# Kernel optimization log

Hardware: AMD Instinct MI355X
Metric: run time of the kernel (lower is better)

Reference implementation:

```python
import jax, jax.numpy as jnp
import numpy as np

N_HEAD = 8
N_HB_TERM = 3


def setup_inputs() -> dict:
    key = jax.random.key(0)
    ks = jax.random.split(key, 6)
    B, N, C, T = 8, 4096, 512, 4096
    s = 0.02  # weight init scale
    return {
        "x": jax.random.normal(ks[0], (B, N, C), jnp.float32),
        "y": jax.random.normal(ks[1], (N_HB_TERM, B, T, C), jnp.float32),
        "Wq": jax.random.normal(ks[2], (C, C), jnp.float32) * s,
        "bq": jnp.zeros((C,), jnp.float32),
        "Wk": jax.random.normal(ks[3], (N_HB_TERM, C, C), jnp.float32) * s,
        "bk": jnp.zeros((N_HB_TERM, C), jnp.float32),
        "Wv": jax.random.normal(ks[4], (N_HB_TERM, C, C), jnp.float32) * s,
        "bv": jnp.zeros((N_HB_TERM, C), jnp.float32),
        "Wp": jax.random.normal(ks[5], (C, C), jnp.float32) * s,
        "bp": jnp.zeros((C,), jnp.float32),
    }


def _heads(t, B, T, H, d):
    # (B, T, C) -> (B, H, T, d)
    return t.reshape(B, T, H, d).transpose(0, 2, 1, 3)


def reference(x, y, Wq, bq, Wk, bk, Wv, bv, Wp, bp):
    B, N, C = x.shape
    H = N_HEAD
    d = C // H
    # query projection + softmax feature map over head dim
    q = _heads(x @ Wq.T + bq, B, N, H, d)          # (B,H,N,d)
    q = jax.nn.softmax(q, axis=-1)
    out = q  # faithful to original: out initialized to q
    for i in range(N_HB_TERM):
        yi = y[i]                                   # (B,T,C)
        T = yi.shape[1]
        k = _heads(yi @ Wk[i].T + bk[i], B, T, H, d)
        v = _heads(yi @ Wv[i].T + bv[i], B, T, H, d)
        k = jax.nn.softmax(k, axis=-1)
        k_cumsum = k.sum(axis=-2, keepdims=True)    # (B,H,1,d)
        D_inv = 1.0 / (q * k_cumsum).sum(axis=-1, keepdims=True)  # (B,H,N,1)
        ctx = jnp.einsum('bhtd,bhte->bhde', k, v)   # (B,H,d,d) small context
        out = out + jnp.einsum('bhnd,bhde->bhne', q, ctx) * D_inv
    out = out.transpose(0, 2, 1, 3).reshape(B, N, C)  # b h n d -> b n (h d)
    return out @ Wp.T + bp
```

## Files before the change

### kernel.cpp

```cpp
#include <hip/hip_runtime.h>


#define B_  8
#define N_  4096
#define C_  512
#define T_  4096
#define H_  8
#define M_  (B_*N_)

typedef __bf16 bf16_8 __attribute__((ext_vector_type(8)));
typedef __bf16 bf16_4 __attribute__((ext_vector_type(4)));
typedef float  f32_4  __attribute__((ext_vector_type(4)));

__device__ __forceinline__ unsigned short f2bf(float f) {
  unsigned u = __float_as_uint(f);
  unsigned r = 0x7FFFu + ((u >> 16) & 1u);
  return (unsigned short)((u + r) >> 16);
}

__device__ __forceinline__ void gload16(const void* g, void* l) {
  __builtin_amdgcn_global_load_lds(
      (const __attribute__((address_space(1))) unsigned int*)g,
      (__attribute__((address_space(3))) unsigned int*)l, 16, 0, 0);
}

__device__ __forceinline__ bf16_8 cvt8(float4 a, float4 b) {
  bf16_8 v;
  v[0]=(__bf16)a.x; v[1]=(__bf16)a.y; v[2]=(__bf16)a.z; v[3]=(__bf16)a.w;
  v[4]=(__bf16)b.x; v[5]=(__bf16)b.y; v[6]=(__bf16)b.z; v[7]=(__bf16)b.w;
  return v;
}

__global__ __launch_bounds__(256) void cvt_f32_bf16(
    const float* __restrict__ in, unsigned short* __restrict__ out, long n4)
{
  long i = (long)blockIdx.x * blockDim.x + threadIdx.x;
  long stride = (long)gridDim.x * blockDim.x;
  for (; i < n4; i += stride) {
    float4 v = ((const float4*)in)[i];
    ushort4 o;
    o.x = f2bf(v.x); o.y = f2bf(v.y); o.z = f2bf(v.z); o.w = f2bf(v.w);
    ((ushort4*)out)[i] = o;
  }
}

__global__ __launch_bounds__(256) void cvt_weights(
    const float* __restrict__ Wq, const float* __restrict__ Wk,
    const float* __restrict__ Wv, const float* __restrict__ Wp,
    unsigned short* __restrict__ wb)
{
  const size_t WCC = (size_t)C_*C_;
  const float* src; unsigned short* dst; long n4;
  switch (blockIdx.y) {
    case 0: src = Wq; dst = wb;         n4 = WCC/4;   break;
    case 1: src = Wk; dst = wb + WCC;   n4 = 3*WCC/4; break;
    case 2: src = Wv; dst = wb + 4*WCC; n4 = 3*WCC/4; break;
    default:src = Wp; dst = wb + 7*WCC; n4 = WCC/4;   break;
  }
  long i = (long)blockIdx.x * blockDim.x + threadIdx.x;
  long stride = (long)gridDim.x * blockDim.x;
  for (; i < n4; i += stride) {
    float4 v = ((const float4*)src)[i];
    ushort4 o;
    o.x = f2bf(v.x); o.y = f2bf(v.y); o.z = f2bf(v.z); o.w = f2bf(v.w);
    ((ushort4*)dst)[i] = o;
  }
}

template<int EPI, int ADT>
__global__ __launch_bounds__(256, 2) void gemm_all(
    const void* __restrict__ Av,
    const unsigned short* __restrict__ Bw,
    const float* __restrict__ bias,
    void* __restrict__ outp)
{
  __shared__ char smem[65536];

  const int tid = threadIdx.x, lane = tid & 63, wid = tid >> 6;
  const int wr = wid >> 1, wc = wid & 1;
  const int l15 = lane & 15, l16 = lane >> 4;
  const size_t row0 = (size_t)blockIdx.x * 128;
  const int col0 = blockIdx.y * 128;

  f32_4 acc[4][4] = {};
  float4 ra[4][2];

  auto load_a = [&](int k0) {
#pragma unroll
    for (int j = 0; j < 4; ++j) {
      int cc = j*256 + tid, row = cc >> 3, s = cc & 7;
      const float* src = (const float*)Av + (row0 + row)*512 + k0 + s*8;
      ra[j][0] = *(const float4*)src;
      ra[j][1] = *(const float4*)(src + 4);
    }
  };
  auto write_a = [&](int bsel) {
    unsigned short* dst = (unsigned short*)smem;
#pragma unroll
    for (int j = 0; j < 4; ++j) {
      int cc = j*256 + tid, row = cc >> 3, s = cc & 7;
      *(bf16_8*)&dst[bsel*8192 + row*64 + ((s ^ (row & 7)) << 3)] = cvt8(ra[j][0], ra[j][1]);
    }
  };
  auto stage_a16 = [&](int k0, int bsel) {
#pragma unroll
    for (int j = 0; j < 4; ++j) {
      int cc = j*256 + tid, row = cc >> 3, s = cc & 7;
      gload16((const unsigned short*)Av + (row0 + row)*512 + k0 + ((s ^ (row & 7)) << 3),
              smem + bsel*16384 + (size_t)(j*256 + wid*64)*16);
    }
  };
  auto stage_b = [&](int k0, int bsel) {
#pragma unroll
    for (int j = 0; j < 4; ++j) {
      int cc = j*256 + tid, row = cc >> 3, s = cc & 7;
      gload16(Bw + (size_t)(col0 + row)*512 + k0 + ((s ^ (row & 7)) << 3),
              smem + 32768 + bsel*16384 + (size_t)(j*256 + wid*64)*16);
    }
  };

  if constexpr (ADT == 0) { load_a(0); stage_b(0, 0); write_a(0); }
  else                    { stage_a16(0, 0); stage_b(0, 0); }
  __syncthreads();
  for (int t = 0; t < 8; ++t) {
    int cur = t & 1;
    if (t < 7) {
      if constexpr (ADT == 0) load_a((t+1)*64);
      else                    stage_a16((t+1)*64, cur ^ 1);
      stage_b((t+1)*64, cur ^ 1);
    }
    const unsigned short* sA = (const unsigned short*)(smem + cur*16384);
    const unsigned short* sB = (const unsigned short*)(smem + 32768 + cur*16384);
#pragma unroll
    for (int kk = 0; kk < 64; kk += 32) {
      bf16_8 af[4], bfr[4];
#pragma unroll
      for (int mi = 0; mi < 4; ++mi) {
        int r = wr*64 + mi*16 + l15;
        int ch = (kk >> 3) + l16;
        af[mi] = *(const bf16_8*)&sA[r*64 + ((ch ^ (r & 7)) << 3)];
      }
#pragma unroll
      for (int ni = 0; ni < 4; ++ni) {
        int r = wc*64 + ni*16 + l15;
        int ch = (kk >> 3) + l16;
        bfr[ni] = *(const bf16_8*)&sB[r*64 + ((ch ^ (r & 7)) << 3)];
      }
#pragma unroll
      for (int mi = 0; mi < 4; ++mi)
#pragma unroll
        for (int ni = 0; ni < 4; ++ni)
          acc[mi][ni] = __builtin_amdgcn_mfma_f32_16x16x32_bf16(af[mi], bfr[ni], acc[mi][ni], 0, 0, 0);
    }
    if (t < 7) { if constexpr (ADT == 0) write_a(cur ^ 1); }
    __syncthreads();
  }

  if constexpr (EPI == 0) {
    float* Cf = (float*)outp;
#pragma unroll
    for (int mi = 0; mi < 4; ++mi) {
      int rb = wr*64 + mi*16 + l16*4;
#pragma unroll
      for (int ni = 0; ni < 4; ++ni) {
        int col = col0 + wc*64 + ni*16 + l15;
        float bv = bias[col];
#pragma unroll
        for (int jj = 0; jj < 4; ++jj)
          Cf[(row0 + rb + jj)*512 + col] = acc[mi][ni][jj] + bv;
      }
    }
  } else {
    unsigned short* ob = (unsigned short*)outp;
    float bvv[4];
#pragma unroll
    for (int ni = 0; ni < 4; ++ni) bvv[ni] = bias[col0 + wc*64 + ni*16 + l15];
    unsigned short* sE = (unsigned short*)smem;
#pragma unroll
    for (int mi = 0; mi < 4; ++mi) {
#pragma unroll
      for (int jj = 0; jj < 4; ++jj) {
        float x[4];
        float s = 0.f;
#pragma unroll
        for (int ni = 0; ni < 4; ++ni) {
          x[ni] = __expf(acc[mi][ni][jj] + bvv[ni]);
          s += x[ni];
        }
#pragma unroll
        for (int o = 8; o; o >>= 1) s += __shfl_xor(s, o);
        float inv = 1.0f / s;
        int r = wr*64 + mi*16 + l16*4 + jj;
#pragma unroll
        for (int ni = 0; ni < 4; ++ni) {
          __bf16 h = (__bf16)(x[ni] * inv);
          sE[r*136 + wc*64 + ni*16 + l15] = *(unsigned short*)&h;
        }
      }
    }
    __syncthreads();
    int r = tid >> 1, seg = tid & 1;
    unsigned short* orow = ob + (row0 + r)*512 + col0 + seg*64;
#pragma unroll
    for (int u = 0; u < 8; ++u)
      *(uint4*)(orow + u*8) = *(const uint4*)&sE[r*136 + seg*64 + u*8];
  }
}

__global__ __launch_bounds__(256, 2) void kvctx_kernel(
    const unsigned short* __restrict__ yb_all,
    const unsigned short* __restrict__ wk_all,
    const unsigned short* __restrict__ wv_all,
    const float* __restrict__ bk_all,
    const float* __restrict__ bv_all,
    float* __restrict__ part,
    float* __restrict__ kcp)
{
  __shared__ char smem[65536];
  unsigned short* sKT = (unsigned short*)smem;
  unsigned short* sVT = (unsigned short*)(smem + 17408);

  const int tid = threadIdx.x, lane = tid & 63, wid = tid >> 6;
  const int wr = wid >> 1, wc = wid & 1;
  const int l15 = lane & 15, l16 = lane >> 4;
  const int gx = blockIdx.x, i = blockIdx.z;
  const int h = gx >> 6, bx = gx & 63;
  const int b = bx >> 3, sub = bx & 7;
  const int bh = b*8 + h;

  const unsigned short* yb = yb_all + (size_t)i*M_*512;
  const unsigned short* Wk_b = wk_all + (size_t)i*512*512 + (size_t)h*64*512;
  const unsigned short* Wv_b = wv_all + (size_t)i*512*512 + (size_t)h*64*512;
  const float* bk = bk_all + i*512 + h*64;
  const float* bv = bv_all + i*512 + h*64;

  f32_4 cacc[2][2] = {};
  float kcp_r[4] = {0.f, 0.f, 0.f, 0.f};

  for (int chunk = 0; chunk < 4; ++chunk) {
    const size_t row0 = (size_t)bx*512 + chunk*128;
    f32_4 acc[4][4] = {};

    auto stage = [&](int k0, int bsel) {
#pragma unroll
      for (int j = 0; j < 4; ++j) {
        int cc = j*256 + tid, row = cc >> 3, s = cc & 7;
        gload16(yb + (row0 + row)*512 + k0 + ((s ^ (row & 7)) << 3),
                smem + bsel*16384 + (size_t)(j*256 + wid*64)*16);
        const unsigned short* wsrc = (j < 2)
            ? Wk_b + (size_t)row*512
            : Wv_b + (size_t)(row - 64)*512;
        gload16(wsrc + k0 + ((s ^ (row & 7)) << 3),
                smem + 32768 + bsel*16384 + (size_t)(j*256 + wid*64)*16);
      }
    };

    stage(0, 0);
    __syncthreads();
    for (int t = 0; t < 8; ++t) {
      int cur = t & 1;
      if (t < 7) stage((t+1)*64, cur ^ 1);
      const unsigned short* sA = (const unsigned short*)(smem + cur*16384);
      const unsigned short* sB = (const unsigned short*)(smem + 32768 + cur*16384);
#pragma unroll
      for (int kk = 0; kk < 64; kk += 32) {
        bf16_8 af[4], bfr[4];
#pragma unroll
        for (int mi = 0; mi < 4; ++mi) {
          int r = wr*64 + mi*16 + l15;
          int ch = (kk >> 3) + l16;
          af[mi] = *(const bf16_8*)&sA[r*64 + ((ch ^ (r & 7)) << 3)];
        }
#pragma unroll
        for (int ni = 0; ni < 4; ++ni) {
          int r = wc*64 + ni*16 + l15;
          int ch = (kk >> 3) + l16;
          bfr[ni] = *(const bf16_8*)&sB[r*64 + ((ch ^ (r & 7)) << 3)];
        }
#pragma unroll
        for (int mi = 0; mi < 4; ++mi)
#pragma unroll
          for (int ni = 0; ni < 4; ++ni)
            acc[mi][ni] = __builtin_amdgcn_mfma_f32_16x16x32_bf16(af[mi], bfr[ni], acc[mi][ni], 0, 0, 0);
      }
      __syncthreads();
    }

    if (wc == 0) {
      float bkv[4];
#pragma unroll
      for (int ni = 0; ni < 4; ++ni) bkv[ni] = bk[ni*16 + l15];
#pragma unroll
      for (int mi = 0; mi < 4; ++mi) {
        float kv[4][4];
#pragma unroll
        for (int jj = 0; jj < 4; ++jj) {
          float s = 0.f;
#pragma unroll
          for (int ni = 0; ni < 4; ++ni) {
            kv[jj][ni] = __expf(acc[mi][ni][jj] + bkv[ni]);
            s += kv[jj][ni];
          }
#pragma unroll
          for (int o = 8; o; o >>= 1) s += __shfl_xor(s, o);
          float inv = 1.0f / s;
#pragma unroll
          for (int ni = 0; ni < 4; ++ni) kv[jj][ni] *= inv;
        }
        int r0 = wr*64 + mi*16 + l16*4;
#pragma unroll
        for (int ni = 0; ni < 4; ++ni) {
          kcp_r[ni] += (kv[0][ni] + kv[1][ni]) + (kv[2][ni] + kv[3][ni]);
          bf16_4 p;
#pragma unroll
          for (int jj = 0; jj < 4; ++jj) p[jj] = (__bf16)kv[jj][ni];
          *(bf16_4*)&sKT[(ni*16 + l15)*136 + r0] = p;
        }
      }
    } else {
      float bvv[4];
#pragma unroll
      for (int ni = 0; ni < 4; ++ni) bvv[ni] = bv[ni*16 + l15];
#pragma unroll
      for (int mi = 0; mi < 4; ++mi) {
        int r0 = wr*64 + mi*16 + l16*4;
#pragma unroll
        for (int ni = 0; ni < 4; ++ni) {
          bf16_4 p;
#pragma unroll
          for (int jj = 0; jj < 4; ++jj) p[jj] = (__bf16)(acc[mi][ni][jj] + bvv[ni]);
          *(bf16_4*)&sVT[(ni*16 + l15)*136 + r0] = p;
        }
      }
    }
    __syncthreads();

#pragma unroll
    for (int ks = 0; ks < 4; ++ks) {
      bf16_8 a2[2], b2[2];
#pragma unroll
      for (int mi = 0; mi < 2; ++mi)
        a2[mi] = *(const bf16_8*)&sKT[(wr*32 + mi*16 + l15)*136 + ks*32 + l16*8];
#pragma unroll
      for (int ni = 0; ni < 2; ++ni)
        b2[ni] = *(const bf16_8*)&sVT[(wc*32 + ni*16 + l15)*136 + ks*32 + l16*8];
#pragma unroll
      for (int mi = 0; mi < 2; ++mi)
#pragma unroll
        for (int ni = 0; ni < 2; ++ni)
          cacc[mi][ni] = __builtin_amdgcn_mfma_f32_16x16x32_bf16(a2[mi], b2[ni], cacc[mi][ni], 0, 0, 0);
    }
    __syncthreads();
  }

  const size_t slot = (size_t)(i*64 + bh)*8 + sub;
  if (wc == 0) {
#pragma unroll
    for (int ni = 0; ni < 4; ++ni) {
      float s = kcp_r[ni];
      s += __shfl_xor(s, 16);
      s += __shfl_xor(s, 32);
      if (l16 == 0) kcp[(slot*2 + wr)*64 + ni*16 + l15] = s;
    }
  }
  float* pb = part + slot*4096;
#pragma unroll
  for (int mi = 0; mi < 2; ++mi)
#pragma unroll
    for (int ni = 0; ni < 2; ++ni) {
      int e0 = wr*32 + mi*16 + l16*4;
      int dv = wc*32 + ni*16 + l15;
      *(f32_4*)&pb[dv*64 + e0] = cacc[mi][ni];
    }
}

__global__ __launch_bounds__(256) void ctx_reduce(
    const float* __restrict__ part,
    const float* __restrict__ kcp,
    float* __restrict__ ctxT,
    float* __restrict__ kc)
{
  int g = blockIdx.x;
  const float* p = part + (size_t)g*8*4096;
  float* o = ctxT + (size_t)g*4096;
#pragma unroll
  for (int jj = 0; jj < 4; ++jj) {
    int j = (jj*256 + threadIdx.x)*4;
    f32_4 s = {};
#pragma unroll
    for (int r = 0; r < 8; ++r) {
      f32_4 v = *(const f32_4*)&p[(size_t)r*4096 + j];
      s[0] += v[0]; s[1] += v[1]; s[2] += v[2]; s[3] += v[3];
    }
    *(f32_4*)&o[j] = s;
  }
  if (threadIdx.x < 64) {
    const float* pk = kcp + (size_t)g*16*64;
    float s = 0.f;
#pragma unroll
    for (int r = 0; r < 16; ++r) s += pk[r*64 + threadIdx.x];
    kc[(size_t)g*64 + threadIdx.x] = s;
  }
}

__global__ __launch_bounds__(256) void combine2(
    const unsigned short* __restrict__ qb,
    const float* __restrict__ ctxT,
    const float* __restrict__ kc,
    unsigned short* __restrict__ outp)
{
  __shared__ unsigned short sQ[128*64];
  __shared__ unsigned short sB[208*64];
  __shared__ float sS[128*3];
  const int tid = threadIdx.x, lane = tid & 63, wid = tid >> 6;
  const int l15 = lane & 15, l16 = lane >> 4;
  const int bh = blockIdx.y, b = bh >> 3, h = bh & 7;
  const int n0 = blockIdx.x * 128;
  const size_t qbase = ((size_t)b*N_ + n0)*C_ + h*64;

#pragma unroll
  for (int j = 0; j < 4; ++j) {
    int c = j*256 + tid;
    int row = c >> 3, c8 = c & 7;
    gload16(qb + qbase + (size_t)row*C_ + c8*8, sQ + (size_t)(j*256 + wid*64)*8);
  }
  for (int f = tid; f < 208*64; f += 256) {
    int col = f >> 6, e = f & 63;
    float val = 0.f;
    if (col < 192)
      val = ctxT[(((size_t)(col >> 6)*64 + bh)*64 + (col & 63))*64 + e];
    else if (col < 195)
      val = kc[((size_t)(col - 192)*64 + bh)*64 + e];
    __bf16 hv = (__bf16)val;
    sB[col*64 + e] = *(unsigned short*)&hv;
  }
  __syncthreads();

  f32_4 acc[2][13] = {};
#pragma unroll
  for (int ks = 0; ks < 2; ++ks) {
    bf16_8 af[2];
#pragma unroll
    for (int mi = 0; mi < 2; ++mi)
      af[mi] = *(const bf16_8*)&sQ[(wid*32 + mi*16 + l15)*64 + ks*32 + l16*8];
#pragma unroll
    for (int ni = 0; ni < 13; ++ni) {
      bf16_8 bfr = *(const bf16_8*)&sB[(ni*16 + l15)*64 + ks*32 + l16*8];
#pragma unroll
      for (int mi = 0; mi < 2; ++mi)
        acc[mi][ni] = __builtin_amdgcn_mfma_f32_16x16x32_bf16(af[mi], bfr, acc[mi][ni], 0, 0, 0);
    }
  }

  if (l15 < 3) {
#pragma unroll
    for (int mi = 0; mi < 2; ++mi)
#pragma unroll
      for (int jj = 0; jj < 4; ++jj)
        sS[(wid*32 + mi*16 + l16*4 + jj)*3 + l15] = acc[mi][12][jj];
  }
  __syncthreads();

#pragma unroll
  for (int mi = 0; mi < 2; ++mi) {
#pragma unroll
    for (int jj = 0; jj < 4; ++jj) {
      int r = wid*32 + mi*16 + l16*4 + jj;
      float inv[3];
#pragma unroll
      for (int i = 0; i < 3; ++i) inv[i] = 1.0f / sS[r*3 + i];
#pragma unroll
      for (int ni = 0; ni < 4; ++ni) {
        int dv = ni*16 + l15;
        unsigned short qh = sQ[r*64 + dv];
        float val = __uint_as_float(((unsigned)qh) << 16);
#pragma unroll
        for (int i = 0; i < 3; ++i) val += acc[mi][i*4 + ni][jj] * inv[i];
        __bf16 hv = (__bf16)val;
        outp[qbase + (size_t)r*C_ + dv] = *(unsigned short*)&hv;
      }
    }
  }
}

extern "C" void kernel_launch(void* const* d_in, const int* in_sizes, int n_in,
                              void* d_out, int out_size, void* d_ws, size_t ws_size,
                              hipStream_t stream)
{
  const float* x  = (const float*)d_in[0];
  const float* y  = (const float*)d_in[1];
  const float* Wq = (const float*)d_in[2];
  const float* bq = (const float*)d_in[3];
  const float* Wk = (const float*)d_in[4];
  const float* bk = (const float*)d_in[5];
  const float* Wv = (const float*)d_in[6];
  const float* bv = (const float*)d_in[7];
  const float* Wp = (const float*)d_in[8];
  const float* bp = (const float*)d_in[9];
  float* out = (float*)d_out;
  char* ws = (char*)d_ws;

  const size_t SZ_BF = (size_t)M_ * C_ * 2;
  const size_t WCC   = (size_t)C_ * C_;

  unsigned short* yb   = (unsigned short*)(ws);
  unsigned short* qb   = (unsigned short*)(ws + 3*SZ_BF);
  unsigned short* kb   = (unsigned short*)(ws + 4*SZ_BF);
  unsigned short* wb   = (unsigned short*)(ws + 5*SZ_BF);
  unsigned short* wq_b = wb;
  unsigned short* wk_b = wb + WCC;
  unsigned short* wv_b = wb + 4*WCC;
  unsigned short* wp_b = wb + 7*WCC;
  float* ctxT = (float*)(wb + 8*WCC);
  float* kc   = ctxT + (size_t)3*64*64*64;

  float* part  = (float*)kb;
  float* kcpar = part + (size_t)192*8*4096;

  cvt_weights<<<dim3(128, 4), 256, 0, stream>>>(Wq, Wk, Wv, Wp, wb);
  cvt_f32_bf16<<<2048, 256, 0, stream>>>(y, yb, (long)3*M_*C_/4);

  gemm_all<1,0><<<dim3(M_/128, 4), 256, 0, stream>>>(x, wq_b, bq, qb);

  kvctx_kernel<<<dim3(512, 1, 3), 256, 0, stream>>>(
      yb, wk_b, wv_b, bk, bv, part, kcpar);
  ctx_reduce<<<192, 256, 0, stream>>>(part, kcpar, ctxT, kc);

  combine2<<<dim3(32, 64), 256, 0, stream>>>(qb, ctxT, kc, kb);
  gemm_all<0,1><<<dim3(M_/128, 4), 256, 0, stream>>>(kb, wp_b, bp, out);
}
```

Measured before the change: 378.0 us.

## Merge conversion kernels and co-schedule Q projection with KV context kernel

Folds the weight and y fp32-to-bf16 conversions into one launch. The Q-projection GEMM and the per-term K/V context kernel now run as a single grid, split by blockIdx.z, so their blocks can occupy the GPU together instead of running back to back. This is meant to cut launch overhead and the tail idle time between dependent launches. The cost is a heavier kernel whose register and LDS use is set by the larger branch, and weight conversion blocks now loop over a wider grid.

```diff
diff --git a/kernel.cpp b/kernel.cpp
--- a/kernel.cpp
+++ b/kernel.cpp
@@ -31,31 +31,21 @@
   return v;
 }
 
-__global__ __launch_bounds__(256) void cvt_f32_bf16(
-    const float* __restrict__ in, unsigned short* __restrict__ out, long n4)
-{
-  long i = (long)blockIdx.x * blockDim.x + threadIdx.x;
-  long stride = (long)gridDim.x * blockDim.x;
-  for (; i < n4; i += stride) {
-    float4 v = ((const float4*)in)[i];
-    ushort4 o;
-    o.x = f2bf(v.x); o.y = f2bf(v.y); o.z = f2bf(v.z); o.w = f2bf(v.w);
-    ((ushort4*)out)[i] = o;
-  }
-}
-
-__global__ __launch_bounds__(256) void cvt_weights(
+__global__ __launch_bounds__(256) void cvt_all(
     const float* __restrict__ Wq, const float* __restrict__ Wk,
     const float* __restrict__ Wv, const float* __restrict__ Wp,
-    unsigned short* __restrict__ wb)
+    const float* __restrict__ y,
+    unsigned short* __restrict__ wb,
+    unsigned short* __restrict__ yb)
 {
   const size_t WCC = (size_t)C_*C_;
   const float* src; unsigned short* dst; long n4;
   switch (blockIdx.y) {
-    case 0: src = Wq; dst = wb;         n4 = WCC/4;   break;
-    case 1: src = Wk; dst = wb + WCC;   n4 = 3*WCC/4; break;
-    case 2: src = Wv; dst = wb + 4*WCC; n4 = 3*WCC/4; break;
-    default:src = Wp; dst = wb + 7*WCC; n4 = WCC/4;   break;
+    case 0: src = Wq; dst = wb;         n4 = WCC/4;          break;
+    case 1: src = Wk; dst = wb + WCC;   n4 = 3*WCC/4;        break;
+    case 2: src = Wv; dst = wb + 4*WCC; n4 = 3*WCC/4;        break;
+    case 3: src = Wp; dst = wb + 7*WCC; n4 = WCC/4;          break;
+    default: src = y; dst = yb;         n4 = (long)3*M_*C_/4; break;
   }
   long i = (long)blockIdx.x * blockDim.x + threadIdx.x;
   long stride = (long)gridDim.x * blockDim.x;
@@ -67,15 +57,13 @@
   }
 }
 
-template<int EPI, int ADT>
-__global__ __launch_bounds__(256, 2) void gemm_all(
-    const void* __restrict__ Av,
+__global__ __launch_bounds__(256, 2) void gemm_final(
+    const unsigned short* __restrict__ A,
     const unsigned short* __restrict__ Bw,
     const float* __restrict__ bias,
-    void* __restrict__ outp)
+    float* __restrict__ Cf)
 {
   __shared__ char smem[65536];
-
   const int tid = threadIdx.x, lane = tid & 63, wid = tid >> 6;
   const int wr = wid >> 1, wc = wid & 1;
   const int l15 = lane & 15, l16 = lane >> 4;
@@ -83,52 +71,23 @@
   const int col0 = blockIdx.y * 128;
 
   f32_4 acc[4][4] = {};
-  float4 ra[4][2];
-
-  auto load_a = [&](int k0) {
+
+  auto stage = [&](int k0, int bsel) {
 #pragma unroll
     for (int j = 0; j < 4; ++j) {
       int cc = j*256 + tid, row = cc >> 3, s = cc & 7;
-      const float* src = (const float*)Av + (row0 + row)*512 + k0 + s*8;
-      ra[j][0] = *(const float4*)src;
-      ra[j][1] = *(const float4*)(src + 4);
-    }
-  };
-  auto write_a = [&](int bsel) {
-    unsigned short* dst = (unsigned short*)smem;
-#pragma unroll
-    for (int j = 0; j < 4; ++j) {
-      int cc = j*256 + tid, row = cc >> 3, s = cc & 7;
-      *(bf16_8*)&dst[bsel*8192 + row*64 + ((s ^ (row & 7)) << 3)] = cvt8(ra[j][0], ra[j][1]);
-    }
-  };
-  auto stage_a16 = [&](int k0, int bsel) {
-#pragma unroll
-    for (int j = 0; j < 4; ++j) {
-      int cc = j*256 + tid, row = cc >> 3, s = cc & 7;
-      gload16((const unsigned short*)Av + (row0 + row)*512 + k0 + ((s ^ (row & 7)) << 3),
+      gload16(A + (row0 + row)*512 + k0 + ((s ^ (row & 7)) << 3),
               smem + bsel*16384 + (size_t)(j*256 + wid*64)*16);
-    }
-  };
-  auto stage_b = [&](int k0, int bsel) {
-#pragma unroll
-    for (int j = 0; j < 4; ++j) {
-      int cc = j*256 + tid, row = cc >> 3, s = cc & 7;
       gload16(Bw + (size_t)(col0 + row)*512 + k0 + ((s ^ (row & 7)) << 3),
               smem + 32768 + bsel*16384 + (size_t)(j*256 + wid*64)*16);
     }
   };
 
-  if constexpr (ADT == 0) { load_a(0); stage_b(0, 0); write_a(0); }
-  else                    { stage_a16(0, 0); stage_b(0, 0); }
+  stage(0, 0);
   __syncthreads();
   for (int t = 0; t < 8; ++t) {
     int cur = t & 1;
-    if (t < 7) {
-      if constexpr (ADT == 0) load_a((t+1)*64);
-      else                    stage_a16((t+1)*64, cur ^ 1);
-      stage_b((t+1)*64, cur ^ 1);
-    }
+    if (t < 7) stage((t+1)*64, cur ^ 1);
     const unsigned short* sA = (const unsigned short*)(smem + cur*16384);
     const unsigned short* sB = (const unsigned short*)(smem + 32768 + cur*16384);
 #pragma unroll
@@ -152,29 +111,108 @@
         for (int ni = 0; ni < 4; ++ni)
           acc[mi][ni] = __builtin_amdgcn_mfma_f32_16x16x32_bf16(af[mi], bfr[ni], acc[mi][ni], 0, 0, 0);
     }
-    if (t < 7) { if constexpr (ADT == 0) write_a(cur ^ 1); }
     __syncthreads();
   }
 
-  if constexpr (EPI == 0) {
-    float* Cf = (float*)outp;
-#pragma unroll
-    for (int mi = 0; mi < 4; ++mi) {
-      int rb = wr*64 + mi*16 + l16*4;
-#pragma unroll
-      for (int ni = 0; ni < 4; ++ni) {
-        int col = col0 + wc*64 + ni*16 + l15;
-        float bv = bias[col];
-#pragma unroll
-        for (int jj = 0; jj < 4; ++jj)
-          Cf[(row0 + rb + jj)*512 + col] = acc[mi][ni][jj] + bv;
-      }
-    }
-  } else {
-    unsigned short* ob = (unsigned short*)outp;
+#pragma unroll
+  for (int mi = 0; mi < 4; ++mi) {
+    int rb = wr*64 + mi*16 + l16*4;
+#pragma unroll
+    for (int ni = 0; ni < 4; ++ni) {
+      int col = col0 + wc*64 + ni*16 + l15;
+      float bv = bias[col];
+#pragma unroll
+      for (int jj = 0; jj < 4; ++jj)
+        Cf[(row0 + rb + jj)*512 + col] = acc[mi][ni][jj] + bv;
+    }
+  }
+}
+
+__global__ __launch_bounds__(256, 2) void mega_kernel(
+    const float* __restrict__ xf,
+    const unsigned short* __restrict__ wq_b, const float* __restrict__ bq,
+    unsigned short* __restrict__ qb,
+    const unsigned short* __restrict__ yb_all,
+    const unsigned short* __restrict__ wk_all,
+    const unsigned short* __restrict__ wv_all,
+    const float* __restrict__ bk_all, const float* __restrict__ bv_all,
+    float* __restrict__ part, float* __restrict__ kcp)
+{
+  __shared__ char smem[65536];
+  const int tid = threadIdx.x, lane = tid & 63, wid = tid >> 6;
+  const int wr = wid >> 1, wc = wid & 1;
+  const int l15 = lane & 15, l16 = lane >> 4;
+  const int z = blockIdx.z;
+
+  if (z < 2) {
+    const int qidx = z*512 + blockIdx.x;
+    const size_t row0 = (size_t)(qidx & 255) * 128;
+    const int col0 = (qidx >> 8) * 128;
+
+    f32_4 acc[4][4] = {};
+    float4 ra[4][2];
+
+    auto load_a = [&](int k0) {
+#pragma unroll
+      for (int j = 0; j < 4; ++j) {
+        int cc = j*256 + tid, row = cc >> 3, s = cc & 7;
+        const float* src = xf + (row0 + row)*512 + k0 + s*8;
+        ra[j][0] = *(const float4*)src;
+        ra[j][1] = *(const float4*)(src + 4);
+      }
+    };
+    auto write_a = [&](int bsel) {
+      unsigned short* dst = (unsigned short*)smem;
+#pragma unroll
+      for (int j = 0; j < 4; ++j) {
+        int cc = j*256 + tid, row = cc >> 3, s = cc & 7;
+        *(bf16_8*)&dst[bsel*8192 + row*64 + ((s ^ (row & 7)) << 3)] = cvt8(ra[j][0], ra[j][1]);
+      }
+    };
+    auto stage_b = [&](int k0, int bsel) {
+#pragma unroll
+      for (int j = 0; j < 4; ++j) {
+        int cc = j*256 + tid, row = cc >> 3, s = cc & 7;
+        gload16(wq_b + (size_t)(col0 + row)*512 + k0 + ((s ^ (row & 7)) << 3),
+                smem + 32768 + bsel*16384 + (size_t)(j*256 + wid*64)*16);
+      }
+    };
+
+    load_a(0); stage_b(0, 0); write_a(0);
+    __syncthreads();
+    for (int t = 0; t < 8; ++t) {
+      int cur = t & 1;
+      if (t < 7) { load_a((t+1)*64); stage_b((t+1)*64, cur ^ 1); }
+      const unsigned short* sA = (const unsigned short*)(smem + cur*16384);
+      const unsigned short* sB = (const unsigned short*)(smem + 32768 + cur*16384);
+#pragma unroll
+      for (int kk = 0; kk < 64; kk += 32) {
+        bf16_8 af[4], bfr[4];
+#pragma unroll
+        for (int mi = 0; mi < 4; ++mi) {
+          int r = wr*64 + mi*16 + l15;
+          int ch = (kk >> 3) + l16;
+          af[mi] = *(const bf16_8*)&sA[r*64 + ((ch ^ (r & 7)) << 3)];
+        }
+#pragma unroll
+        for (int ni = 0; ni < 4; ++ni) {
+          int r = wc*64 + ni*16 + l15;
+          int ch = (kk >> 3) + l16;
+          bfr[ni] = *(const bf16_8*)&sB[r*64 + ((ch ^ (r & 7)) << 3)];
+        }
+#pragma unroll
+        for (int mi = 0; mi < 4; ++mi)
+#pragma unroll
+          for (int ni = 0; ni < 4; ++ni)
+            acc[mi][ni] = __builtin_amdgcn_mfma_f32_16x16x32_bf16(af[mi], bfr[ni], acc[mi][ni], 0, 0, 0);
+      }
+      if (t < 7) write_a(cur ^ 1);
+      __syncthreads();
+    }
+
     float bvv[4];
 #pragma unroll
-    for (int ni = 0; ni < 4; ++ni) bvv[ni] = bias[col0 + wc*64 + ni*16 + l15];
+    for (int ni = 0; ni < 4; ++ni) bvv[ni] = bq[col0 + wc*64 + ni*16 + l15];
     unsigned short* sE = (unsigned short*)smem;
 #pragma unroll
     for (int mi = 0; mi < 4; ++mi) {
@@ -200,30 +238,17 @@
     }
     __syncthreads();
     int r = tid >> 1, seg = tid & 1;
-    unsigned short* orow = ob + (row0 + r)*512 + col0 + seg*64;
+    unsigned short* orow = qb + (row0 + r)*512 + col0 + seg*64;
 #pragma unroll
     for (int u = 0; u < 8; ++u)
       *(uint4*)(orow + u*8) = *(const uint4*)&sE[r*136 + seg*64 + u*8];
-  }
-}
-
-__global__ __launch_bounds__(256, 2) void kvctx_kernel(
-    const unsigned short* __restrict__ yb_all,
-    const unsigned short* __restrict__ wk_all,
-    const unsigned short* __restrict__ wv_all,
-    const float* __restrict__ bk_all,
-    const float* __restrict__ bv_all,
-    float* __restrict__ part,
-    float* __restrict__ kcp)
-{
-  __shared__ char smem[65536];
+    return;
+  }
+
   unsigned short* sKT = (unsigned short*)smem;
   unsigned short* sVT = (unsigned short*)(smem + 17408);
 
-  const int tid = threadIdx.x, lane = tid & 63, wid = tid >> 6;
-  const int wr = wid >> 1, wc = wid & 1;
-  const int l15 = lane & 15, l16 = lane >> 4;
-  const int gx = blockIdx.x, i = blockIdx.z;
+  const int gx = blockIdx.x, i = z - 2;
   const int h = gx >> 6, bx = gx & 63;
   const int b = bx >> 3, sub = bx & 7;
   const int bh = b*8 + h;
@@ -517,15 +542,12 @@
   float* part  = (float*)kb;
   float* kcpar = part + (size_t)192*8*4096;
 
-  cvt_weights<<<dim3(128, 4), 256, 0, stream>>>(Wq, Wk, Wv, Wp, wb);
-  cvt_f32_bf16<<<2048, 256, 0, stream>>>(y, yb, (long)3*M_*C_/4);
-
-  gemm_all<1,0><<<dim3(M_/128, 4), 256, 0, stream>>>(x, wq_b, bq, qb);
-
-  kvctx_kernel<<<dim3(512, 1, 3), 256, 0, stream>>>(
-      yb, wk_b, wv_b, bk, bv, part, kcpar);
+  cvt_all<<<dim3(2048, 5), 256, 0, stream>>>(Wq, Wk, Wv, Wp, y, wb, yb);
+
+  mega_kernel<<<dim3(512, 1, 5), 256, 0, stream>>>(
+      x, wq_b, bq, qb, yb, wk_b, wv_b, bk, bv, part, kcpar);
   ctx_reduce<<<192, 256, 0, stream>>>(part, kcpar, ctxT, kc);
 
   combine2<<<dim3(32, 64), 256, 0, stream>>>(qb, ctxT, kc, kb);
-  gemm_all<0,1><<<dim3(M_/128, 4), 256, 0, stream>>>(kb, wp_b, bp, out);
-}
+  gemm_final<<<dim3(M_/128, 4), 256, 0, stream>>>(kb, wp_b, bp, out);
+}
```

Measured after the change: 363.7 us (median of 2 runs). 1.04x faster.
